# Kernel tuning notes

Hardware: AMD Instinct MI355X
Metric: run time of the kernel (lower is better)

The kernel has to match this reference:

```python
import jax, jax.numpy as jnp
import numpy as np

T, B, OBS, D, H = 512, 256, 256, 512, 512  # time, batch, obs_dim, embed/gru hidden, critic hidden


def setup_inputs() -> dict:
    key = jax.random.key(0)
    ks = jax.random.split(key, 10)
    s = lambda fan_in: 1.0 / np.sqrt(fan_in)
    return {
        "obs": jax.random.normal(ks[0], (T, B, OBS), dtype=jnp.float32),
        "done": jax.random.bernoulli(ks[1], 0.01, (T, B)),
        "hstate": jnp.zeros((B, D), dtype=jnp.float32),
        # embedding dense
        "W_emb": jax.random.normal(ks[2], (OBS, D), dtype=jnp.float32) * s(OBS),
        "b_emb": jnp.zeros((D,), dtype=jnp.float32),
        # GRU: input kernels [D, 3D] (r|z|n), hidden kernels [D, 3D], input bias [3D], hn bias [D]
        "Wi": jax.random.normal(ks[3], (D, 3 * D), dtype=jnp.float32) * s(D),
        "bi": jnp.zeros((3 * D,), dtype=jnp.float32),
        "Wh": jax.random.normal(ks[4], (D, 3 * D), dtype=jnp.float32) * s(D),
        "bhn": jnp.zeros((D,), dtype=jnp.float32),
        # critic MLP
        "W1": jax.random.normal(ks[5], (D, H), dtype=jnp.float32) * s(D),
        "b1": jnp.zeros((H,), dtype=jnp.float32),
        "W2": jax.random.normal(ks[6], (H, 1), dtype=jnp.float32) * s(H),
        "b2": jnp.zeros((1,), dtype=jnp.float32),
    }


def _forward(obs, done, hstate, W_emb, b_emb, Wi, bi, Wh, bhn, W1, b1, W2, b2):
    # embedding: [T, B, D]
    emb = jax.nn.relu(jnp.einsum("tbo,od->tbd", obs, W_emb) + b_emb)
    # precompute input-side gate preactivations for all timesteps: [T, B, 3D]
    xg = jnp.einsum("tbd,de->tbe", emb, Wi) + bi

    def step(h, inp):
        xg_t, d_t = inp
        # reset carry where episode ended (flax GRU init carry is zeros)
        h = jnp.where(d_t[:, None], 0.0, h)
        hg = h @ Wh  # [B, 3D]
        r = jax.nn.sigmoid(xg_t[:, :D] + hg[:, :D])
        z = jax.nn.sigmoid(xg_t[:, D:2 * D] + hg[:, D:2 * D])
        n = jnp.tanh(xg_t[:, 2 * D:] + r * (hg[:, 2 * D:] + bhn))
        h_new = (1.0 - z) * n + z * h
        return h_new, h_new

    h_last, ys = jax.lax.scan(step, hstate, (xg, done))  # ys: [T, B, D]
    critic = jax.nn.relu(jnp.einsum("tbd,dh->tbh", ys, W1) + b1)
    value = jnp.squeeze(jnp.einsum("tbh,ho->tbo", critic, W2) + b2, axis=-1)  # [T, B]
    return h_last, value


def reference(obs, done, hstate, W_emb, b_emb, Wi, bi, Wh, bhn, W1, b1, W2, b2):
    return _forward(obs, done, hstate, W_emb, b_emb, Wi, bi, Wh, bhn, W1, b1, W2, b2)
```

## Files before the change

kernel.cpp:

```cpp
#include <hip/hip_runtime.h>

#define TT   512
#define BB   256
#define OBSD 256
#define DD   512
#define HH   512
#define MROWS (TT*BB)

typedef __attribute__((ext_vector_type(8))) short short8;
typedef __attribute__((ext_vector_type(4))) float f32x4;

__device__ __forceinline__ ushort f2b(float f){
  unsigned int x = __float_as_uint(f);
  x = (x + 0x7fffu + ((x >> 16) & 1u)) >> 16;
  return (ushort)x;
}
__device__ __forceinline__ float b2f(ushort u){
  return __uint_as_float(((unsigned int)u) << 16);
}
__device__ __forceinline__ float sigm(float x){ return 1.f/(1.f + __expf(-x)); }
__device__ __forceinline__ float tanh_f(float x){ return 1.f - 2.f/(__expf(2.f*x) + 1.f); }

__global__ void k_transpose_bf16(const float* __restrict__ W, ushort* __restrict__ Wt,
                                 int K, int N){
  int i = blockIdx.x*256 + threadIdx.x;
  if(i >= K*N) return;
  int k = i / N, n = i % N;
  Wt[(size_t)n*K + k] = f2b(W[i]);
}

__global__ void k_f32_to_bf16(const float* __restrict__ in, ushort* __restrict__ out,
                              int n4){
  int i = blockIdx.x*256 + threadIdx.x;
  if(i >= n4) return;
  const float4 v = ((const float4*)in)[i];
  union{ ushort u[4]; uint2 d; } p;
  p.u[0] = f2b(v.x); p.u[1] = f2b(v.y); p.u[2] = f2b(v.z); p.u[3] = f2b(v.w);
  ((uint2*)out)[i] = p.d;
}

__global__ void k_detect(const int* __restrict__ done, int* __restrict__ flag){
  __shared__ int cnt;
  if(threadIdx.x == 0) cnt = 0;
  __syncthreads();
  int c = 0;
  for(int i = threadIdx.x; i < 32768; i += 256) c += (done[i] != 0);
  for(int off = 32; off; off >>= 1) c += __shfl_down(c, off, 64);
  if((threadIdx.x & 63) == 0) atomicAdd(&cnt, c);
  __syncthreads();
  if(threadIdx.x == 0) *flag = (cnt > 700) ? 1 : 0;
}

#define GSTAGE(buf, k0v) { \
  _Pragma("unroll") \
  for(int j = 0; j < 2; j++){ \
    const int flat = tid*16 + j*4096;         \
    const int rw  = flat >> 6;                \
    const int ke  = (flat & 63) >> 1;         \
    __builtin_amdgcn_global_load_lds( \
      (const __attribute__((address_space(1))) void*)(A + (m0+rw)*(size_t)K + (k0v) + ke), \
      (__attribute__((address_space(3))) void*)((char*)As[buf] + flat), 16, 0, 0); \
    __builtin_amdgcn_global_load_lds( \
      (const __attribute__((address_space(1))) void*)(Bt + (n0+rw)*(size_t)K + (k0v) + ke), \
      (__attribute__((address_space(3))) void*)((char*)Bs[buf] + flat), 16, 0, 0); \
  } }
#define GCOMPUTE(buf) { \
    short8 af[4], bf[4]; \
    _Pragma("unroll") for(int mi=0;mi<4;mi++) \
      af[mi] = *(const short8*)((const char*)As[buf] + (wr*64+mi*16+l16)*64 + l4*16); \
    _Pragma("unroll") for(int ni=0;ni<4;ni++) \
      bf[ni] = *(const short8*)((const char*)Bs[buf] + (wc*64+ni*16+l16)*64 + l4*16); \
    _Pragma("unroll") for(int mi=0;mi<4;mi++) \
      _Pragma("unroll") for(int ni=0;ni<4;ni++) \
        acc[mi][ni] = __builtin_amdgcn_mfma_f32_16x16x32_bf16(af[mi], bf[ni], acc[mi][ni], 0,0,0); }

__global__ __launch_bounds__(256) void k_gemm128(const ushort* __restrict__ A,
                                                 const ushort* __restrict__ Bt,
                                                 const float* __restrict__ bias,
                                                 ushort* __restrict__ C,
                                                 int M, int N, int K, int relu,
                                                 int xg_layout){
  __shared__ __align__(16) ushort As[2][4096];
  __shared__ __align__(16) ushort Bs[2][4096];
  const int tid = threadIdx.x;
  const int l = tid & 63, l16 = l & 15, l4 = l >> 4;
  const int w = tid >> 6, wr = w >> 1, wc = w & 1;
  const size_t m0 = (size_t)blockIdx.x*128, n0 = (size_t)blockIdx.y*128;
  f32x4 acc[4][4] = {};

  GSTAGE(0, 0);
  asm volatile("s_waitcnt vmcnt(0)" ::: "memory");
  __syncthreads();
  int cur = 0;
  for(int k0 = 32; k0 < K; k0 += 32){
    GSTAGE(cur^1, k0);
    GCOMPUTE(cur);
    asm volatile("s_waitcnt vmcnt(0)" ::: "memory");
    __syncthreads();
    cur ^= 1;
  }
  GCOMPUTE(cur);

  #pragma unroll
  for(int ni=0;ni<4;ni++){
    const int col = (int)n0 + wc*64 + ni*16 + l16;
    const float bv = bias[col];
    #pragma unroll
    for(int mi=0;mi<4;mi++){
      #pragma unroll
      for(int r=0;r<4;r++){
        const int row = (int)m0 + wr*64 + mi*16 + l4*4 + r;
        float v = acc[mi][ni][r] + bv;
        if(relu) v = fmaxf(v, 0.f);
        size_t addr;
        if(xg_layout){
          const int tl = row >> 8, brow = row & 255;
          const int gg = brow >> 5, r32 = brow & 31;
          const int gate = col >> 9, cw = col & 511, ds2 = cw >> 4, c16 = cw & 15;
          addr = ((((size_t)tl*32 + ds2)*8 + gg)*3 + gate)*512 + r32*16 + c16;
        } else {
          addr = (size_t)row*N + col;
        }
        C[addr] = f2b(v);
      }
    }
  }
}

__device__ __forceinline__ void flag_barrier(int* cntbase, int g, int ds, int target,
                                             int tid){
  asm volatile("s_waitcnt vmcnt(0)" ::: "memory");
  __syncthreads();
  if(tid == 0)
    __hip_atomic_store(cntbase + g*32 + ds, target,
                       __ATOMIC_RELAXED, __HIP_MEMORY_SCOPE_AGENT);
  if(tid < 32){
    const int* fp = cntbase + g*32 + tid;
    while(__hip_atomic_load(fp, __ATOMIC_RELAXED, __HIP_MEMORY_SCOPE_AGENT) < target)
      __builtin_amdgcn_s_sleep(1);
  }
  __syncthreads();
}

#define ALD2(v, j) { const ushort* pj_ = hgrp + (j)*1024; \
  asm volatile("global_load_dwordx4 %0, %1, off sc0 sc1" : "=&v"(v) : "v"(pj_)); }

__global__ __launch_bounds__(128, 1) void k_scan_coop(
    const ushort* __restrict__ xg,
    const void* __restrict__ donep,
    const int* __restrict__ flagp, const float* __restrict__ h_in,
    const ushort* __restrict__ WhT, const float* __restrict__ bhn,
    ushort* __restrict__ ys, float* __restrict__ h_io,
    float* __restrict__ h_last, ushort* __restrict__ hbf,
    int t0, int steps, int* __restrict__ cntbase){
  __shared__ __align__(16) ushort whs[48*512];
  __shared__ __align__(16) ushort xgs[2][1536];
  __shared__ unsigned char dns[512*32];
  const int tid = threadIdx.x;
  const int m = tid >> 6, l = tid & 63, l16 = l & 15, l4 = l >> 4;
  const int bid = blockIdx.x;
  const int g = bid >> 5, ds = bid & 31;
  const int use8 = *flagp;
  const unsigned char* d8 = (const unsigned char*)donep;
  const int* d32 = (const int*)donep;

  for(int e = tid; e < 3072; e += 128){
    const int lr = e >> 6;
    const int kc = (e & 63) << 3;
    const int grow_w = (lr >> 4)*DD + ds*16 + (lr & 15);
    short8 v = *(const short8*)(WhT + (size_t)grow_w*DD + kc);
    int boff = ((lr << 10) + (kc << 1)) ^ ((lr & 7) << 4);
    *(short8*)((char*)whs + boff) = v;
  }
  for(int e = tid; e < steps*32; e += 128){
    const int tloc = e >> 5, r = e & 31;
    const int gi = (t0 + tloc)*BB + g*32 + r;
    dns[e] = use8 ? (d8[gi] != 0) : (d32[gi] != 0);
  }

  const int r32 = m*16 + l16;
  const int row = g*32 + r32;
  const int d0  = ds*16 + l4*4;
  const float4 bh4 = *(const float4*)(bhn + d0);

  float hf[4];
  {
    const float4 hv4 = *(const float4*)(h_in + (size_t)row*DD + d0);
    hf[0]=hv4.x; hf[1]=hv4.y; hf[2]=hv4.z; hf[3]=hv4.w;
    union{ ushort u[4]; uint2 v; } p;
    #pragma unroll
    for(int r=0;r<4;r++) p.u[r] = f2b(hf[r]);
    const ushort* pp = hbf + (size_t)g*16384 + ds*512 + r32*16 + l4*4;
    asm volatile("global_store_dwordx2 %0, %1, off sc0 sc1" :: "v"(pp), "v"(p.v) : "memory");
  }
  {
    const ushort* sl = xg + (((size_t)0*32 + ds)*8 + g)*1536;
    __builtin_amdgcn_global_load_lds(
      (const __attribute__((address_space(1))) void*)(sl + m*512 + l*8),
      (__attribute__((address_space(3))) void*)(&xgs[0][m*512]), 16, 0, 0);
    if(m == 0)
      __builtin_amdgcn_global_load_lds(
        (const __attribute__((address_space(1))) void*)(sl + 1024 + l*8),
        (__attribute__((address_space(3))) void*)(&xgs[0][1024]), 16, 0, 0);
  }
  flag_barrier(cntbase, g, ds, 1, tid);

  int rb[3], sw[3];
  #pragma unroll
  for(int gi=0; gi<3; gi++){
    const int lr = gi*16 + l16;
    rb[gi] = lr << 10;
    sw[gi] = (lr & 7) << 4;
  }
  const ushort* hb0 = hbf;
  const ushort* hb1 = hbf + (size_t)BB*DD;
  const size_t csub = (size_t)((l4>>1) << 9) + (size_t)r32*16 + ((l4&1) << 3);
  int cur = 0;

  for(int tl = 0; tl < steps; tl++){
    const ushort* hcur = (tl & 1) ? hb1 : hb0;
    ushort* hnxt = (ushort*)((tl & 1) ? hb0 : hb1);
    const bool dn = dns[tl*32 + r32];

    if(tl + 1 < steps){
      const int nb = cur ^ 1;
      const ushort* sl = xg + (((size_t)(tl+1)*32 + ds)*8 + g)*1536;
      __builtin_amdgcn_global_load_lds(
        (const __attribute__((address_space(1))) void*)(sl + m*512 + l*8),
        (__attribute__((address_space(3))) void*)(&xgs[nb][m*512]), 16, 0, 0);
      if(m == 0)
        __builtin_amdgcn_global_load_lds(
          (const __attribute__((address_space(1))) void*)(sl + 1024 + l*8),
          (__attribute__((address_space(3))) void*)(&xgs[nb][1024]), 16, 0, 0);
    }

    const ushort* hgrp = hcur + (size_t)g*16384 + csub;
    short8 a0,a1,a2,a3,a4,a5,a6,a7,a8,a9,a10,a11,a12,a13,a14,a15;
    ALD2(a0,0);   ALD2(a1,1);   ALD2(a2,2);   ALD2(a3,3);
    ALD2(a4,4);   ALD2(a5,5);   ALD2(a6,6);   ALD2(a7,7);
    ALD2(a8,8);   ALD2(a9,9);   ALD2(a10,10); ALD2(a11,11);
    ALD2(a12,12); ALD2(a13,13); ALD2(a14,14); ALD2(a15,15);
    asm volatile("s_waitcnt vmcnt(0)" ::: "memory");
    __builtin_amdgcn_sched_barrier(0);

    if(__builtin_expect(dn, 0)){
      const short8 z = {0,0,0,0,0,0,0,0};
      a0=z;a1=z;a2=z;a3=z;a4=z;a5=z;a6=z;a7=z;
      a8=z;a9=z;a10=z;a11=z;a12=z;a13=z;a14=z;a15=z;
    }

    f32x4 acc[3] = {};
    #define STEPK(ak, k0lit) { \
      const int kboff = ((k0lit + l4*8) << 1); \
      _Pragma("unroll") \
      for(int gi=0; gi<3; gi++){ \
        const short8 wf = *(const short8*)((const char*)whs + ((rb[gi] + kboff) ^ sw[gi])); \
        acc[gi] = __builtin_amdgcn_mfma_f32_16x16x32_bf16(wf, ak, acc[gi], 0, 0, 0); \
      } }
    STEPK(a0,0)    STEPK(a1,32)   STEPK(a2,64)   STEPK(a3,96)
    STEPK(a4,128)  STEPK(a5,160)  STEPK(a6,192)  STEPK(a7,224)
    STEPK(a8,256)  STEPK(a9,288)  STEPK(a10,320) STEPK(a11,352)
    STEPK(a12,384) STEPK(a13,416) STEPK(a14,448) STEPK(a15,480)
    #undef STEPK

    union{ ushort u[4]; uint2 v; } p;
    {
      const uint2 xru = *(const uint2*)&xgs[cur][        r32*16 + l4*4];
      const uint2 xzu = *(const uint2*)&xgs[cur][ 512 +  r32*16 + l4*4];
      const uint2 xnu = *(const uint2*)&xgs[cur][1024 +  r32*16 + l4*4];
      const ushort xr4[4] = {(ushort)(xru.x&0xffff),(ushort)(xru.x>>16),
                             (ushort)(xru.y&0xffff),(ushort)(xru.y>>16)};
      const ushort xz4[4] = {(ushort)(xzu.x&0xffff),(ushort)(xzu.x>>16),
                             (ushort)(xzu.y&0xffff),(ushort)(xzu.y>>16)};
      const ushort xn4[4] = {(ushort)(xnu.x&0xffff),(ushort)(xnu.x>>16),
                             (ushort)(xnu.y&0xffff),(ushort)(xnu.y>>16)};
      const float bhv[4] = {bh4.x, bh4.y, bh4.z, bh4.w};
      #pragma unroll
      for(int r=0;r<4;r++){
        const float hold = dn ? 0.f : hf[r];
        const float rg = sigm(b2f(xr4[r]) + acc[0][r]);
        const float zg = sigm(b2f(xz4[r]) + acc[1][r]);
        const float ng = tanh_f(b2f(xn4[r]) + rg*(acc[2][r] + bhv[r]));
        const float hv = (1.f - zg)*ng + zg*hold;
        hf[r] = hv;
        p.u[r] = f2b(hv);
      }
      const ushort* pp = hnxt + (size_t)g*16384 + ds*512 + r32*16 + l4*4;
      asm volatile("global_store_dwordx2 %0, %1, off sc0 sc1" :: "v"(pp), "v"(p.v) : "memory");
    }
    flag_barrier(cntbase, g, ds, tl + 2, tid);
    *(uint2*)(ys + ((size_t)tl*BB + row)*DD + d0) = p.v;
    cur ^= 1;
  }

  {
    float4 o; o.x=hf[0]; o.y=hf[1]; o.z=hf[2]; o.w=hf[3];
    *(float4*)(h_io   + (size_t)row*DD + d0) = o;
    *(float4*)(h_last + (size_t)row*DD + d0) = o;
  }
}

__global__ __launch_bounds__(1024) void k_scan(const ushort* __restrict__ xg,
                                               const void* __restrict__ donep,
                                               const int* __restrict__ flagp,
                                               const float* __restrict__ h_in,
                                               const ushort* __restrict__ WhT,
                                               const float* __restrict__ bhn,
                                               ushort* __restrict__ ys,
                                               float* __restrict__ h_io,
                                               float* __restrict__ h_last,
                                               int t0, int steps){
  __shared__ __align__(16) float  h_f[16][DD];
  __shared__ __align__(16) ushort h_b[16][DD];
  const int tid = threadIdx.x;
  const int w = tid >> 6, l = tid & 63, l16 = l & 15, l4 = l >> 4;
  const int b0 = blockIdx.x * 16;
  const int use8 = *flagp;
  const unsigned char* d8 = (const unsigned char*)donep;
  const int* d32 = (const int*)donep;

  for(int e = tid; e < 16*DD; e += 1024){
    int b = e >> 9, dd = e & (DD-1);
    float v = h_in[(size_t)(b0 + b)*DD + dd];
    h_f[b][dd] = v; h_b[b][dd] = f2b(v);
  }
  __syncthreads();

  const int dbase = w * 32;
  const ushort* bp[6];
  #pragma unroll
  for(int g=0; g<3; g++)
    #pragma unroll
    for(int nt=0; nt<2; nt++)
      bp[g*2+nt] = WhT + (size_t)(g*DD + dbase + nt*16 + l16) * DD;

  for(int tl = 0; tl < steps; tl++){
    const int drow = (t0 + tl)*BB + b0;
    const bool dnA = use8 ? (d8[drow + l16] != 0) : (d32[drow + l16] != 0);
    f32x4 acc[3][2] = {};
    const short8 zf = {0,0,0,0,0,0,0,0};
    for(int k0 = 0; k0 < DD; k0 += 32){
      const int kb = k0 + l4*8;
      short8 a = *(const short8*)&h_b[l16][kb];
      if(dnA) a = zf;
      #pragma unroll
      for(int g=0; g<3; g++)
        #pragma unroll
        for(int nt=0; nt<2; nt++){
          const short8 b = *(const short8*)(bp[g*2+nt] + kb);
          acc[g][nt] = __builtin_amdgcn_mfma_f32_16x16x32_bf16(a, b, acc[g][nt], 0, 0, 0);
        }
    }
    float hnew[2][4];
    #pragma unroll
    for(int nt=0; nt<2; nt++){
      const int dd = dbase + nt*16 + l16;
      const float bh = bhn[dd];
      const int ds2 = dd >> 4, c16 = dd & 15;
      #pragma unroll
      for(int r=0; r<4; r++){
        const int brow = l4*4 + r;
        const int grow = b0 + brow;
        const int gg = grow >> 5, r32 = grow & 31;
        const bool dn = use8 ? (d8[drow + brow] != 0) : (d32[drow + brow] != 0);
        const size_t sbase = (((size_t)tl*32 + ds2)*8 + gg)*1536 + r32*16 + c16;
        const float xr = b2f(xg[sbase]);
        const float xz = b2f(xg[sbase + 512]);
        const float xn = b2f(xg[sbase + 1024]);
        const float hold = dn ? 0.f : h_f[brow][dd];
        const float rg = sigm(xr + acc[0][nt][r]);
        const float zg = sigm(xz + acc[1][nt][r]);
        const float ng = tanh_f(xn + rg*(acc[2][nt][r] + bh));
        hnew[nt][r] = (1.f - zg)*ng + zg*hold;
      }
    }
    __syncthreads();
    #pragma unroll
    for(int nt=0; nt<2; nt++){
      const int dd = dbase + nt*16 + l16;
      #pragma unroll
      for(int r=0; r<4; r++){
        const int brow = l4*4 + r;
        const size_t rowl = (size_t)(tl*BB + b0 + brow);
        const float hv = hnew[nt][r];
        h_f[brow][dd] = hv;
        h_b[brow][dd] = f2b(hv);
        ys[rowl*DD + dd] = f2b(hv);
      }
    }
    __syncthreads();
  }

  for(int e = tid; e < 16*DD; e += 1024){
    int b = e >> 9, dd = e & (DD-1);
    float v = h_f[b][dd];
    h_io[(size_t)(b0 + b)*DD + dd] = v;
    h_last[(size_t)(b0 + b)*DD + dd] = v;
  }
}

__global__ __launch_bounds__(256) void k_value(const ushort* __restrict__ critic,
                                               const float* __restrict__ W2,
                                               const float* __restrict__ b2,
                                               float* __restrict__ val){
  const int w = threadIdx.x >> 6, l = threadIdx.x & 63;
  const size_t row = (size_t)blockIdx.x*4 + w;
  const ushort* cp = critic + row*HH + l*8;
  const float* wp = W2 + l*8;
  float s = 0.f;
  #pragma unroll
  for(int j=0;j<8;j++) s += b2f(cp[j]) * wp[j];
  for(int off=32; off; off>>=1) s += __shfl_down(s, off, 64);
  if(l == 0) val[row] = s + b2[0];
}

extern "C" void kernel_launch(void* const* d_in, const int* in_sizes, int n_in,
                              void* d_out, int out_size, void* d_ws, size_t ws_size,
                              hipStream_t stream){
  const float* obs    = (const float*)d_in[0];
  const void*  done   = d_in[1];
  const float* hstate = (const float*)d_in[2];
  const float* W_emb  = (const float*)d_in[3];
  const float* b_emb  = (const float*)d_in[4];
  const float* Wi     = (const float*)d_in[5];
  const float* bi     = (const float*)d_in[6];
  const float* Wh     = (const float*)d_in[7];
  const float* bhn    = (const float*)d_in[8];
  const float* W1     = (const float*)d_in[9];
  const float* b1     = (const float*)d_in[10];
  const float* W2     = (const float*)d_in[11];
  const float* b2     = (const float*)d_in[12];
  float* out = (float*)d_out;
  char*  ws  = (char*)d_ws;

  ushort* WembT = (ushort*)(ws + 0);
  ushort* WiT   = (ushort*)(ws + 262144);
  ushort* WhT   = (ushort*)(ws + 1835008);
  ushort* W1T   = (ushort*)(ws + 3407872);
  int*    flag  = (int*)   (ws + 3932160);
  float*  hio   = (float*) (ws + 3936256);
  ushort* hbf   = (ushort*)(ws + 4460544);
  int*    cnt   = (int*)   (ws + 4984832);
  const size_t FIX = 5242880;

  int TC = 0;
  {
    const int cands[6] = {512, 256, 128, 64, 32, 16};
    for(int i = 0; i < 6; i++){
      size_t need = FIX + (size_t)cands[i] * 1310720u;
      if(need <= ws_size){ TC = cands[i]; break; }
    }
  }
  if(TC == 0) return;

  ushort* emb_c  = (ushort*)(ws + FIX);
  ushort* xg_c   = (ushort*)(ws + FIX + (size_t)TC*262144u);
  ushort* ys_c   = (ushort*)(ws + FIX + (size_t)TC*1048576u);
  ushort* crit_c = emb_c;
  ushort* obs_bf = ys_c;

  k_transpose_bf16<<<(OBSD*DD+255)/256, 256, 0, stream>>>(W_emb, WembT, OBSD, DD);
  k_transpose_bf16<<<(DD*3*DD+255)/256, 256, 0, stream>>>(Wi, WiT, DD, 3*DD);
  k_transpose_bf16<<<(DD*3*DD+255)/256, 256, 0, stream>>>(Wh, WhT, DD, 3*DD);
  k_transpose_bf16<<<(DD*HH+255)/256, 256, 0, stream>>>(W1, W1T, DD, HH);
  k_detect<<<1, 256, 0, stream>>>((const int*)done, flag);

  const int nchunks = TT / TC;
  for(int c = 0; c < nchunks; c++){
    const int Mc = TC * BB;
    const size_t row0 = (size_t)c * Mc;
    k_f32_to_bf16<<<(Mc*OBSD/4 + 255)/256, 256, 0, stream>>>(obs + row0*OBSD, obs_bf,
                                                             Mc*OBSD/4);
    k_gemm128<<<dim3(Mc/128, DD/128), 256, 0, stream>>>(obs_bf, WembT, b_emb,
                                                        emb_c, Mc, DD, OBSD, 1, 0);
    k_gemm128<<<dim3(Mc/128, (3*DD)/128), 256, 0, stream>>>(emb_c, WiT, bi,
                                                            xg_c, Mc, 3*DD, DD, 0, 1);
    {
      const ushort* xg_a = xg_c;  const void* done_a = done;
      const int* flag_a = flag;   const float* hin_a = (c == 0) ? hstate : hio;
      const ushort* wht_a = WhT;  const float* bhn_a = bhn;
      ushort* ys_a = ys_c;        float* hio_a = hio;
      float* hl_a = out;          ushort* hbf_a = hbf;
      int t0_a = c*TC;            int steps_a = TC;
      int* cnt_a = cnt;
      void* args[13] = { (void*)&xg_a, (void*)&done_a, (void*)&flag_a, (void*)&hin_a,
                         (void*)&wht_a, (void*)&bhn_a, (void*)&ys_a, (void*)&hio_a,
                         (void*)&hl_a, (void*)&hbf_a, (void*)&t0_a, (void*)&steps_a,
                         (void*)&cnt_a };
      hipMemsetAsync(cnt, 0, 32768, stream);
      hipError_t err = hipLaunchCooperativeKernel((const void*)k_scan_coop,
                                                  dim3(256), dim3(128), args, 0, stream);
      if(err != hipSuccess){
        k_scan<<<16, 1024, 0, stream>>>(xg_c, done, flag, hin_a, WhT, bhn,
                                        ys_c, hio, out, c*TC, TC);
      }
    }
    k_gemm128<<<dim3(Mc/128, HH/128), 256, 0, stream>>>(ys_c, W1T, b1,
                                                        crit_c, Mc, HH, DD, 1, 0);
    k_value<<<Mc/4, 256, 0, stream>>>(crit_c, W2, b2, out + (size_t)BB*DD + row0);
  }
}
```

Measured before the change: 2.999 ms.

## Use XCC-local fast barrier and cached hidden-state loads when group shares an XCC

Block-to-(group, d-slice) mapping changes so each group's 32 blocks are strided across block IDs, in the hope that round-robin dispatch puts a whole group on one XCC. Each block records its XCC ID, and if every block in the group sits on the same XCC, the scan uses a fast path. That path uses non-coherent (L2-cached) hidden-state loads and stores plus an atomic-based barrier with a periodic fallback check, avoiding system-coherent sc0/sc1 traffic each step. The risk is correctness if the XCC-locality assumption or the cache invalidation is wrong; otherwise it falls back to the old slow barrier path.

```diff
diff --git a/kernel.cpp b/kernel.cpp
--- a/kernel.cpp
+++ b/kernel.cpp
@@ -127,23 +127,94 @@
   }
 }
 
-__device__ __forceinline__ void flag_barrier(int* cntbase, int g, int ds, int target,
-                                             int tid){
+__device__ __forceinline__ void bar_slow(int* cntA, int g, int ds, int target, int tid){
   asm volatile("s_waitcnt vmcnt(0)" ::: "memory");
   __syncthreads();
   if(tid == 0)
-    __hip_atomic_store(cntbase + g*32 + ds, target,
+    __hip_atomic_store(cntA + g*32 + ds, target,
                        __ATOMIC_RELAXED, __HIP_MEMORY_SCOPE_AGENT);
   if(tid < 32){
-    const int* fp = cntbase + g*32 + tid;
+    const int* fp = cntA + g*32 + tid;
     while(__hip_atomic_load(fp, __ATOMIC_RELAXED, __HIP_MEMORY_SCOPE_AGENT) < target)
       __builtin_amdgcn_s_sleep(1);
   }
   __syncthreads();
 }
 
-#define ALD2(v, j) { const ushort* pj_ = hgrp + (j)*1024; \
+__device__ __forceinline__ void bar_fast(int* cntL, int* cntA, int g, int ds,
+                                         int target, int tid){
+  asm volatile("s_waitcnt vmcnt(0)" ::: "memory");
+  __syncthreads();
+  if(tid == 0){
+    int* pL = cntL + g*32 + ds;
+    asm volatile("global_atomic_swap %0, %1, off" :: "v"(pL), "v"(target) : "memory");
+    __hip_atomic_store(cntA + g*32 + ds, target,
+                       __ATOMIC_RELAXED, __HIP_MEMORY_SCOPE_AGENT);
+  }
+  if(tid < 32){
+    int* fpL = cntL + g*32 + tid;
+    const int* fpA = cntA + g*32 + tid;
+    int it = 0;
+    for(;;){
+      int old;
+      asm volatile("global_atomic_add %0, %1, %2, off sc0"
+                   : "=v"(old) : "v"(fpL), "v"(0) : "memory");
+      asm volatile("s_waitcnt vmcnt(0)" ::: "memory");
+      if(old >= target) break;
+      if((++it & 15) == 0 &&
+         __hip_atomic_load(fpA, __ATOMIC_RELAXED, __HIP_MEMORY_SCOPE_AGENT) >= target)
+        break;
+      __builtin_amdgcn_s_sleep(1);
+    }
+  }
+  __syncthreads();
+  asm volatile("buffer_inv sc0" ::: "memory");
+}
+
+#define ALD_S(v, j) { const ushort* pj_ = hgrp + (j)*1024; \
   asm volatile("global_load_dwordx4 %0, %1, off sc0 sc1" : "=&v"(v) : "v"(pj_)); }
+#define ALD_F(v, j) { const ushort* pj_ = hgrp + (j)*1024; \
+  asm volatile("global_load_dwordx4 %0, %1, off" : "=&v"(v) : "v"(pj_)); }
+#define DECL_A short8 a0,a1,a2,a3,a4,a5,a6,a7,a8,a9,a10,a11,a12,a13,a14,a15
+#define ALOADS(M) M(a0,0);M(a1,1);M(a2,2);M(a3,3);M(a4,4);M(a5,5);M(a6,6);M(a7,7); \
+  M(a8,8);M(a9,9);M(a10,10);M(a11,11);M(a12,12);M(a13,13);M(a14,14);M(a15,15)
+#define ZERO_A { const short8 z = {0,0,0,0,0,0,0,0}; \
+  a0=z;a1=z;a2=z;a3=z;a4=z;a5=z;a6=z;a7=z;a8=z;a9=z;a10=z;a11=z;a12=z;a13=z;a14=z;a15=z; }
+#define STEPK(ak, k0lit) { const int kboff = ((k0lit + l4*8) << 1); \
+  _Pragma("unroll") for(int gi=0; gi<3; gi++){ \
+    const short8 wf = *(const short8*)((const char*)whs + ((rb[gi] + kboff) ^ sw[gi])); \
+    acc[gi] = __builtin_amdgcn_mfma_f32_16x16x32_bf16(wf, ak, acc[gi], 0, 0, 0); } }
+#define MFMA48 STEPK(a0,0) STEPK(a1,32) STEPK(a2,64) STEPK(a3,96) STEPK(a4,128) \
+  STEPK(a5,160) STEPK(a6,192) STEPK(a7,224) STEPK(a8,256) STEPK(a9,288) STEPK(a10,320) \
+  STEPK(a11,352) STEPK(a12,384) STEPK(a13,416) STEPK(a14,448) STEPK(a15,480)
+#define XG_PREFETCH(tls, nb) { \
+  const ushort* sl = xg + (((size_t)(tls)*32 + ds)*8 + g)*1536; \
+  __builtin_amdgcn_global_load_lds( \
+    (const __attribute__((address_space(1))) void*)(sl + m*512 + l*8), \
+    (__attribute__((address_space(3))) void*)(&xgs[nb][m*512]), 16, 0, 0); \
+  if(m == 0) __builtin_amdgcn_global_load_lds( \
+    (const __attribute__((address_space(1))) void*)(sl + 1024 + l*8), \
+    (__attribute__((address_space(3))) void*)(&xgs[nb][1024]), 16, 0, 0); }
+#define GRU_EPI(pv) { \
+  const uint2 xru = *(const uint2*)&xgs[cur][        r32*16 + l4*4]; \
+  const uint2 xzu = *(const uint2*)&xgs[cur][ 512 +  r32*16 + l4*4]; \
+  const uint2 xnu = *(const uint2*)&xgs[cur][1024 +  r32*16 + l4*4]; \
+  const ushort xr4[4] = {(ushort)(xru.x&0xffff),(ushort)(xru.x>>16), \
+                         (ushort)(xru.y&0xffff),(ushort)(xru.y>>16)}; \
+  const ushort xz4[4] = {(ushort)(xzu.x&0xffff),(ushort)(xzu.x>>16), \
+                         (ushort)(xzu.y&0xffff),(ushort)(xzu.y>>16)}; \
+  const ushort xn4[4] = {(ushort)(xnu.x&0xffff),(ushort)(xnu.x>>16), \
+                         (ushort)(xnu.y&0xffff),(ushort)(xnu.y>>16)}; \
+  const float bhv[4] = {bh4.x, bh4.y, bh4.z, bh4.w}; \
+  union{ ushort u[4]; uint2 v; } p; \
+  _Pragma("unroll") for(int r=0;r<4;r++){ \
+    const float hold = dn ? 0.f : hf[r]; \
+    const float rg = sigm(b2f(xr4[r]) + acc[0][r]); \
+    const float zg = sigm(b2f(xz4[r]) + acc[1][r]); \
+    const float ng = tanh_f(b2f(xn4[r]) + rg*(acc[2][r] + bhv[r])); \
+    const float hv = (1.f - zg)*ng + zg*hold; \
+    hf[r] = hv; p.u[r] = f2b(hv); } \
+  pv = p.v; }
 
 __global__ __launch_bounds__(128, 1) void k_scan_coop(
     const ushort* __restrict__ xg,
@@ -152,17 +223,20 @@
     const ushort* __restrict__ WhT, const float* __restrict__ bhn,
     ushort* __restrict__ ys, float* __restrict__ h_io,
     float* __restrict__ h_last, ushort* __restrict__ hbf,
-    int t0, int steps, int* __restrict__ cntbase){
+    int t0, int steps, int* __restrict__ cntbase, int* __restrict__ xcc_tab){
   __shared__ __align__(16) ushort whs[48*512];
   __shared__ __align__(16) ushort xgs[2][1536];
   __shared__ unsigned char dns[512*32];
+  __shared__ int fastf;
   const int tid = threadIdx.x;
   const int m = tid >> 6, l = tid & 63, l16 = l & 15, l4 = l >> 4;
   const int bid = blockIdx.x;
-  const int g = bid >> 5, ds = bid & 31;
+  const int g = bid & 7, ds = bid >> 3;
   const int use8 = *flagp;
   const unsigned char* d8 = (const unsigned char*)donep;
   const int* d32 = (const int*)donep;
+  int* cntL = cntbase;
+  int* cntA = cntbase + 256;
 
   for(int e = tid; e < 3072; e += 128){
     const int lr = e >> 6;
@@ -193,17 +267,28 @@
     const ushort* pp = hbf + (size_t)g*16384 + ds*512 + r32*16 + l4*4;
     asm volatile("global_store_dwordx2 %0, %1, off sc0 sc1" :: "v"(pp), "v"(p.v) : "memory");
   }
+  XG_PREFETCH(0, 0);
+  int my_xcc;
+  asm volatile("s_getreg_b32 %0, hwreg(HW_REG_XCC_ID)" : "=s"(my_xcc));
+  if(tid == 0){
+    int* p = xcc_tab + bid;
+    asm volatile("global_store_dword %0, %1, off sc0 sc1" :: "v"(p), "v"(my_xcc) : "memory");
+  }
+  bar_slow(cntA, g, ds, 1, tid);
   {
-    const ushort* sl = xg + (((size_t)0*32 + ds)*8 + g)*1536;
-    __builtin_amdgcn_global_load_lds(
-      (const __attribute__((address_space(1))) void*)(sl + m*512 + l*8),
-      (__attribute__((address_space(3))) void*)(&xgs[0][m*512]), 16, 0, 0);
-    if(m == 0)
-      __builtin_amdgcn_global_load_lds(
-        (const __attribute__((address_space(1))) void*)(sl + 1024 + l*8),
-        (__attribute__((address_space(3))) void*)(&xgs[0][1024]), 16, 0, 0);
-  }
-  flag_barrier(cntbase, g, ds, 1, tid);
+    int bad = 0;
+    if(tid < 32){
+      const int* p = xcc_tab + tid*8 + g;
+      int v;
+      asm volatile("global_load_dword %0, %1, off sc0 sc1" : "=v"(v) : "v"(p) : "memory");
+      asm volatile("s_waitcnt vmcnt(0)" ::: "memory");
+      bad = (v != my_xcc);
+    }
+    const int anybad = __any(bad);
+    if(tid == 0) fastf = !anybad;
+    __syncthreads();
+  }
+  const int fast = fastf;
 
   int rb[3], sw[3];
   #pragma unroll
@@ -217,80 +302,51 @@
   const size_t csub = (size_t)((l4>>1) << 9) + (size_t)r32*16 + ((l4&1) << 3);
   int cur = 0;
 
-  for(int tl = 0; tl < steps; tl++){
-    const ushort* hcur = (tl & 1) ? hb1 : hb0;
-    ushort* hnxt = (ushort*)((tl & 1) ? hb0 : hb1);
-    const bool dn = dns[tl*32 + r32];
-
-    if(tl + 1 < steps){
-      const int nb = cur ^ 1;
-      const ushort* sl = xg + (((size_t)(tl+1)*32 + ds)*8 + g)*1536;
-      __builtin_amdgcn_global_load_lds(
-        (const __attribute__((address_space(1))) void*)(sl + m*512 + l*8),
-        (__attribute__((address_space(3))) void*)(&xgs[nb][m*512]), 16, 0, 0);
-      if(m == 0)
-        __builtin_amdgcn_global_load_lds(
-          (const __attribute__((address_space(1))) void*)(sl + 1024 + l*8),
-          (__attribute__((address_space(3))) void*)(&xgs[nb][1024]), 16, 0, 0);
-    }
-
-    const ushort* hgrp = hcur + (size_t)g*16384 + csub;
-    short8 a0,a1,a2,a3,a4,a5,a6,a7,a8,a9,a10,a11,a12,a13,a14,a15;
-    ALD2(a0,0);   ALD2(a1,1);   ALD2(a2,2);   ALD2(a3,3);
-    ALD2(a4,4);   ALD2(a5,5);   ALD2(a6,6);   ALD2(a7,7);
-    ALD2(a8,8);   ALD2(a9,9);   ALD2(a10,10); ALD2(a11,11);
-    ALD2(a12,12); ALD2(a13,13); ALD2(a14,14); ALD2(a15,15);
-    asm volatile("s_waitcnt vmcnt(0)" ::: "memory");
-    __builtin_amdgcn_sched_barrier(0);
-
-    if(__builtin_expect(dn, 0)){
-      const short8 z = {0,0,0,0,0,0,0,0};
-      a0=z;a1=z;a2=z;a3=z;a4=z;a5=z;a6=z;a7=z;
-      a8=z;a9=z;a10=z;a11=z;a12=z;a13=z;a14=z;a15=z;
-    }
-
-    f32x4 acc[3] = {};
-    #define STEPK(ak, k0lit) { \
-      const int kboff = ((k0lit + l4*8) << 1); \
-      _Pragma("unroll") \
-      for(int gi=0; gi<3; gi++){ \
-        const short8 wf = *(const short8*)((const char*)whs + ((rb[gi] + kboff) ^ sw[gi])); \
-        acc[gi] = __builtin_amdgcn_mfma_f32_16x16x32_bf16(wf, ak, acc[gi], 0, 0, 0); \
-      } }
-    STEPK(a0,0)    STEPK(a1,32)   STEPK(a2,64)   STEPK(a3,96)
-    STEPK(a4,128)  STEPK(a5,160)  STEPK(a6,192)  STEPK(a7,224)
-    STEPK(a8,256)  STEPK(a9,288)  STEPK(a10,320) STEPK(a11,352)
-    STEPK(a12,384) STEPK(a13,416) STEPK(a14,448) STEPK(a15,480)
-    #undef STEPK
-
-    union{ ushort u[4]; uint2 v; } p;
-    {
-      const uint2 xru = *(const uint2*)&xgs[cur][        r32*16 + l4*4];
-      const uint2 xzu = *(const uint2*)&xgs[cur][ 512 +  r32*16 + l4*4];
-      const uint2 xnu = *(const uint2*)&xgs[cur][1024 +  r32*16 + l4*4];
-      const ushort xr4[4] = {(ushort)(xru.x&0xffff),(ushort)(xru.x>>16),
-                             (ushort)(xru.y&0xffff),(ushort)(xru.y>>16)};
-      const ushort xz4[4] = {(ushort)(xzu.x&0xffff),(ushort)(xzu.x>>16),
-                             (ushort)(xzu.y&0xffff),(ushort)(xzu.y>>16)};
-      const ushort xn4[4] = {(ushort)(xnu.x&0xffff),(ushort)(xnu.x>>16),
-                             (ushort)(xnu.y&0xffff),(ushort)(xnu.y>>16)};
-      const float bhv[4] = {bh4.x, bh4.y, bh4.z, bh4.w};
-      #pragma unroll
-      for(int r=0;r<4;r++){
-        const float hold = dn ? 0.f : hf[r];
-        const float rg = sigm(b2f(xr4[r]) + acc[0][r]);
-        const float zg = sigm(b2f(xz4[r]) + acc[1][r]);
-        const float ng = tanh_f(b2f(xn4[r]) + rg*(acc[2][r] + bhv[r]));
-        const float hv = (1.f - zg)*ng + zg*hold;
-        hf[r] = hv;
-        p.u[r] = f2b(hv);
-      }
+  if(fast){
+    asm volatile("buffer_inv sc0" ::: "memory");
+    for(int tl = 0; tl < steps; tl++){
+      const ushort* hcur = (tl & 1) ? hb1 : hb0;
+      ushort* hnxt = (ushort*)((tl & 1) ? hb0 : hb1);
+      const bool dn = dns[tl*32 + r32];
+      if(tl + 1 < steps) XG_PREFETCH(tl+1, cur^1);
+      const ushort* hgrp = hcur + (size_t)g*16384 + csub;
+      DECL_A;
+      ALOADS(ALD_F);
+      asm volatile("s_waitcnt vmcnt(0)" ::: "memory");
+      __builtin_amdgcn_sched_barrier(0);
+      if(__builtin_expect(dn, 0)) ZERO_A;
+      f32x4 acc[3] = {};
+      MFMA48;
+      uint2 pv;
+      GRU_EPI(pv);
       const ushort* pp = hnxt + (size_t)g*16384 + ds*512 + r32*16 + l4*4;
-      asm volatile("global_store_dwordx2 %0, %1, off sc0 sc1" :: "v"(pp), "v"(p.v) : "memory");
-    }
-    flag_barrier(cntbase, g, ds, tl + 2, tid);
-    *(uint2*)(ys + ((size_t)tl*BB + row)*DD + d0) = p.v;
-    cur ^= 1;
+      asm volatile("global_store_dwordx2 %0, %1, off" :: "v"(pp), "v"(pv) : "memory");
+      bar_fast(cntL, cntA, g, ds, tl + 2, tid);
+      *(uint2*)(ys + ((size_t)tl*BB + row)*DD + d0) = pv;
+      cur ^= 1;
+    }
+  } else {
+    for(int tl = 0; tl < steps; tl++){
+      const ushort* hcur = (tl & 1) ? hb1 : hb0;
+      ushort* hnxt = (ushort*)((tl & 1) ? hb0 : hb1);
+      const bool dn = dns[tl*32 + r32];
+      if(tl + 1 < steps) XG_PREFETCH(tl+1, cur^1);
+      const ushort* hgrp = hcur + (size_t)g*16384 + csub;
+      DECL_A;
+      ALOADS(ALD_S);
+      asm volatile("s_waitcnt vmcnt(0)" ::: "memory");
+      __builtin_amdgcn_sched_barrier(0);
+      if(__builtin_expect(dn, 0)) ZERO_A;
+      f32x4 acc[3] = {};
+      MFMA48;
+      uint2 pv;
+      GRU_EPI(pv);
+      const ushort* pp = hnxt + (size_t)g*16384 + ds*512 + r32*16 + l4*4;
+      asm volatile("global_store_dwordx2 %0, %1, off sc0 sc1" :: "v"(pp), "v"(pv) : "memory");
+      bar_slow(cntA, g, ds, tl + 2, tid);
+      *(uint2*)(ys + ((size_t)tl*BB + row)*DD + d0) = pv;
+      cur ^= 1;
+    }
   }
 
   {
@@ -441,6 +497,7 @@
   float*  hio   = (float*) (ws + 3936256);
   ushort* hbf   = (ushort*)(ws + 4460544);
   int*    cnt   = (int*)   (ws + 4984832);
+  int*    xcc   = (int*)   (ws + 5017600);
   const size_t FIX = 5242880;
 
   int TC = 0;
@@ -482,12 +539,12 @@
       ushort* ys_a = ys_c;        float* hio_a = hio;
       float* hl_a = out;          ushort* hbf_a = hbf;
       int t0_a = c*TC;            int steps_a = TC;
-      int* cnt_a = cnt;
-      void* args[13] = { (void*)&xg_a, (void*)&done_a, (void*)&flag_a, (void*)&hin_a,
+      int* cnt_a = cnt;           int* xcc_a = xcc;
+      void* args[14] = { (void*)&xg_a, (void*)&done_a, (void*)&flag_a, (void*)&hin_a,
                          (void*)&wht_a, (void*)&bhn_a, (void*)&ys_a, (void*)&hio_a,
                          (void*)&hl_a, (void*)&hbf_a, (void*)&t0_a, (void*)&steps_a,
-                         (void*)&cnt_a };
-      hipMemsetAsync(cnt, 0, 32768, stream);
+                         (void*)&cnt_a, (void*)&xcc_a };
+      hipMemsetAsync(cnt, 0, 4096, stream);
       hipError_t err = hipLaunchCooperativeKernel((const void*)k_scan_coop,
                                                   dim3(256), dim3(128), args, 0, stream);
       if(err != hipSuccess){
```

Result: no change. 2.997 ms (-0.1%).
